# Performance work log

Hardware: AMD Instinct MI355X
Metric: run time of the kernel (lower is better)

## Reference

```python
import jax, jax.numpy as jnp
import numpy as np

B, S, HE, HD = 32, 2048, 1024, 1024

def setup_inputs() -> dict:
    key = jax.random.key(0)
    k1, k2, k3, k4, k5 = jax.random.split(key, 5)
    enc_hiddens = jax.random.normal(k1, (B, S, HE), dtype=jnp.float32)
    dec_hidden = jax.random.normal(k2, (B, HD), dtype=jnp.float32)
    mask = jax.random.randint(k3, (B, S), 0, 2).astype(bool)  # True = masked out
    # params init uniform(-0.05, 0.05) as in init_weights
    W = jax.random.uniform(k4, (HD, HE + HD), dtype=jnp.float32, minval=-0.05, maxval=0.05)
    V = jax.random.uniform(k5, (1, HD), dtype=jnp.float32, minval=-0.05, maxval=0.05)
    return {"enc_hiddens": enc_hiddens, "dec_hidden": dec_hidden, "mask": mask, "W": W, "V": V}

def reference(enc_hiddens, dec_hidden, mask, W, V):
    # e = V^T tanh(W [enc; dec]) -- split W to avoid materializing the concat:
    # W @ [enc;dec] == W_enc @ enc + W_dec @ dec (same math, fused-friendly)
    HE_ = enc_hiddens.shape[-1]
    W_enc, W_dec = W[:, :HE_], W[:, HE_:]
    h = jnp.tanh(jnp.einsum('bse,de->bsd', enc_hiddens, W_enc)
                 + jnp.einsum('be,de->bd', dec_hidden, W_dec)[:, None, :])  # [B,S,HD]
    scores = jnp.einsum('bsd,od->bs', h, V)  # [B,S] (o==1 squeezed)
    scores = jnp.where(mask, -jnp.inf, scores)
    attn = jax.nn.softmax(scores, axis=1)[:, None, :]  # [B,1,S]
    ctx = jnp.einsum('bos,bse->be', attn, enc_hiddens)  # squeeze of bmm -> [B,HE]
    return (ctx, attn)
```

## Files before the change

### kernel.cpp

```cpp
#include <hip/hip_runtime.h>
#include <hip/hip_bf16.h>
#include <math.h>

#define BB 32
#define SS 2048
#define HE 1024
#define HD 1024
#define WROW (HE + HD)

typedef __attribute__((ext_vector_type(8))) short bf16x8;
typedef __attribute__((ext_vector_type(4))) float f32x4;
typedef __attribute__((ext_vector_type(16))) float f32x16;
typedef __attribute__((ext_vector_type(8))) unsigned short u16x8;

__device__ __forceinline__ unsigned short f2bf(float f) {
    union { float f; unsigned u; } v; v.f = f;
    unsigned r = v.u + 0x7fffu + ((v.u >> 16) & 1u);
    return (unsigned short)(r >> 16);
}

__device__ __forceinline__ unsigned int pk2(float x, float y) {
    union { __hip_bfloat162 h; unsigned int u; } c;
    c.h = __float22bfloat162_rn(float2{x, y});
    return c.u;
}

#define LGKM0()  asm volatile("s_waitcnt lgkmcnt(0)" ::: "memory")
#define BAR()    asm volatile("s_barrier" ::: "memory")

__global__ __launch_bounds__(256) void k_cvt_wfrag(const float* __restrict__ W,
                                                   unsigned short* __restrict__ wf) {
    int i = blockIdx.x * 256 + threadIdx.x;
    int d = i >> 7;
    int c = i & 127;
    const float4* src = (const float4*)(W + (size_t)d * WROW + c * 8);
    float4 a = src[0], b2 = src[1];
    u16x8 o;
    o[0] = f2bf(a.x);  o[1] = f2bf(a.y);  o[2] = f2bf(a.z);  o[3] = f2bf(a.w);
    o[4] = f2bf(b2.x); o[5] = f2bf(b2.y); o[6] = f2bf(b2.z); o[7] = f2bf(b2.w);
    int ks = c >> 1;
    int l  = (d & 31) + 32 * (c & 1);
    int g  = d >> 5;
    *(u16x8*)(wf + ((size_t)(g * 64 + ks) * 64 + l) * 8) = o;
}

__global__ __launch_bounds__(256) void k_projdec2(const float* __restrict__ dec,
                                                  const float* __restrict__ W,
                                                  float* __restrict__ proj) {
    const int tid = threadIdx.x;
    const int dl = tid >> 6;
    const int b  = (tid >> 1) & 31;
    const int hf = tid & 1;
    const int d  = blockIdx.x * 4 + dl;
    const float* wrow = W + (size_t)d * WROW + HE + hf * 512;
    const float* dv   = dec + b * HD + hf * 512;
    float s = 0.f;
    #pragma unroll 4
    for (int e = 0; e < 512; e += 4) {
        float4 w4 = *(const float4*)(wrow + e);
        float4 x4 = *(const float4*)(dv + e);
        s += w4.x * x4.x + w4.y * x4.y + w4.z * x4.z + w4.w * x4.w;
    }
    s += __shfl_xor(s, 1, 64);
    if (hf == 0) proj[b * HD + d] = s;
}

__global__ __launch_bounds__(64) void k_compact(const int* __restrict__ mask,
                                                int* __restrict__ idx,
                                                int* __restrict__ cntblk) {
    const int b = blockIdx.x, ln = threadIdx.x;
    int running = 0;
    for (int s0 = 0; s0 < SS; s0 += 64) {
        int m = mask[b * SS + s0 + ln];
        unsigned long long bal = __ballot(m == 0);
        int pos = __popcll(bal & ((1ull << ln) - 1ull));
        if (m == 0) idx[b * SS + running + pos] = s0 + ln;
        running += __popcll(bal);
    }
    int padded = (running + 63) & ~63;
    for (int i = running + ln; i < padded; i += 64) idx[b * SS + i] = (int)0x80000000;
    if (ln == 0) cntblk[b] = padded >> 6;
}

__global__ __launch_bounds__(1024) void k_blocktab(const int* __restrict__ cntblk,
                                                   int* __restrict__ btab) {
    __shared__ int off[33];
    if (threadIdx.x == 0) {
        int a = 0;
        for (int i = 0; i < 32; i++) { off[i] = a; a += cntblk[i]; }
        off[32] = a;
    }
    __syncthreads();
    int j = threadIdx.x, e = -1;
    #pragma unroll
    for (int b2 = 0; b2 < 32; b2++)
        if (j >= off[b2] && j < off[b2 + 1]) e = (b2 << 16) | (j - off[b2]);
    btab[j] = e;
}

__global__ __launch_bounds__(512, 2) void k_scores_mfma8b(
        const float* __restrict__ enc,
        const unsigned short* __restrict__ wf,
        const float* __restrict__ V,
        const float* __restrict__ proj,
        const int* __restrict__ idx,
        const int* __restrict__ btab,
        float* __restrict__ psc) {
    __shared__ unsigned short SM[8192];

    const int ent = btab[blockIdx.x];
    if (ent < 0) return;

    const int tid = threadIdx.x;
    const int wv = tid >> 6, ln = tid & 63, l31 = ln & 31, hi = ln >> 5;
    const int b   = ent >> 16;
    const int lt0 = (ent & 0xffff) << 6;

    const int rid = idx[b * SS + lt0 + (tid >> 3)];
    const size_t arow = ((size_t)b * SS + (rid & 0xffff)) * 1024;

    f32x16 acc[2][4];
    #pragma unroll
    for (int m = 0; m < 2; m++)
        #pragma unroll
        for (int n = 0; n < 4; n++)
            #pragma unroll
            for (int r = 0; r < 16; r++) acc[m][n][r] = 0.f;

    float4 areg[2];
    bf16x8 bgE[8], bgF[8];

    #define LOAD_A(k) do { \
        const float4* g_ = (const float4*)(enc + arow + (k) + (tid & 7) * 8); \
        areg[0] = g_[0]; areg[1] = g_[1]; \
    } while (0)

    #define CVTW_A(buf) do { \
        int row_ = tid >> 3; \
        union { u16x8 s; uint4 u; } pk_; \
        pk_.u.x = pk2(areg[0].x, areg[0].y); \
        pk_.u.y = pk2(areg[0].z, areg[0].w); \
        pk_.u.z = pk2(areg[1].x, areg[1].y); \
        pk_.u.w = pk2(areg[1].z, areg[1].w); \
        *(u16x8*)&SM[(buf) * 4096 + row_ * 64 + (((tid & 7) ^ (row_ & 7)) << 3)] = pk_.s; \
    } while (0)

    #define LOADB(bgx, tt, ksb) do { \
        _Pragma("unroll") \
        for (int kk = 0; kk < 2; kk++) \
            _Pragma("unroll") \
            for (int n = 0; n < 4; n++) \
                bgx[kk * 4 + n] = *(const bf16x8*)(wf + ((size_t)((wv * 4 + n) * 64 + (tt) * 4 + (ksb) + kk) * 64 + ln) * 8); \
        } while (0)

    #define HALF(bg, ksb, Ac) do { \
        _Pragma("unroll") \
        for (int kk = 0; kk < 2; kk++) { \
            bf16x8 af0, af1; \
            { int c_ = ((ksb) + kk) * 2 + hi; int row_ = l31; \
              af0 = *(const bf16x8*)&(Ac)[row_ * 64 + ((c_ ^ (row_ & 7)) << 3)]; } \
            { int c_ = ((ksb) + kk) * 2 + hi; int row_ = 32 + l31; \
              af1 = *(const bf16x8*)&(Ac)[row_ * 64 + ((c_ ^ (row_ & 7)) << 3)]; } \
            __builtin_amdgcn_s_setprio(1); \
            _Pragma("unroll") \
            for (int n = 0; n < 4; n++) \
                acc[0][n] = __builtin_amdgcn_mfma_f32_32x32x16_bf16(af0, bg[kk * 4 + n], acc[0][n], 0, 0, 0); \
            _Pragma("unroll") \
            for (int n = 0; n < 4; n++) \
                acc[1][n] = __builtin_amdgcn_mfma_f32_32x32x16_bf16(af1, bg[kk * 4 + n], acc[1][n], 0, 0, 0); \
            __builtin_amdgcn_s_setprio(0); \
        } } while (0)

    LOADB(bgE, 0, 0); LOADB(bgF, 0, 2);
    LOAD_A(0);
    CVTW_A(0);
    LOAD_A(64);
    LGKM0(); BAR();

    for (int t = 0; t < 16; ++t) {
        const int cur = t & 1, nxt = cur ^ 1;
        const unsigned short* Ac = SM + cur * 4096;

        HALF(bgE, 0, Ac);

        if (t < 15) {
            LOADB(bgE, t + 1, 0);
            CVTW_A(nxt);
            if (t < 14) LOAD_A((t + 2) * 64);
        }

        HALF(bgF, 2, Ac);

        if (t < 15) {
            LOADB(bgF, t + 1, 2);
            LGKM0(); BAR();
        }
    }
    #undef LOAD_A
    #undef CVTW_A
    #undef LOADB
    #undef HALF

    float sc[2][16];
    #pragma unroll
    for (int m = 0; m < 2; m++)
        #pragma unroll
        for (int r = 0; r < 16; r++) sc[m][r] = 0.f;
    #pragma unroll
    for (int n = 0; n < 4; n++) {
        int d = wv * 128 + n * 32 + l31;
        float pd  = proj[b * 1024 + d];
        float vv  = V[d];
        float vv2 = 2.f * vv;
        #pragma unroll
        for (int m = 0; m < 2; m++)
            #pragma unroll
            for (int r = 0; r < 16; r++) {
                float y  = acc[m][n][r] + pd;
                float e2 = __expf(2.f * y);
                float rc = __builtin_amdgcn_rcpf(e2 + 1.f);
                sc[m][r] += vv - vv2 * rc;
            }
    }

    #pragma unroll
    for (int m = 0; m < 2; m++)
        #pragma unroll
        for (int r = 0; r < 16; r++) {
            float v = sc[m][r];
            v += __shfl_xor(v, 1, 64);
            v += __shfl_xor(v, 2, 64);
            v += __shfl_xor(v, 4, 64);
            v += __shfl_xor(v, 8, 64);
            v += __shfl_xor(v, 16, 64);
            sc[m][r] = v;
        }

    __syncthreads();
    float* redf = (float*)SM;
    if (l31 == 0) {
        #pragma unroll
        for (int m = 0; m < 2; m++)
            #pragma unroll
            for (int r = 0; r < 16; r++) {
                int tok = m * 32 + (r & 3) + 8 * (r >> 2) + 4 * hi;
                redf[tok * 8 + wv] = sc[m][r];
            }
    }
    __syncthreads();
    if (tid < 64) {
        float s = 0.f;
        #pragma unroll
        for (int w = 0; w < 8; w++) s += redf[tid * 8 + w];
        int sidx = idx[b * SS + lt0 + tid];
        if (sidx >= 0) psc[b * SS + sidx] = s;
    }
}

__global__ __launch_bounds__(256) void k_softmax_p(const float* __restrict__ psc,
                                                   const int* __restrict__ mask,
                                                   float* __restrict__ attn) {
    __shared__ float sred[256];
    const int b = blockIdx.x, tid = threadIdx.x;
    float vals[8];
    int   msk[8];
    float lmax = -1e30f;
    #pragma unroll
    for (int i = 0; i < 8; i++) {
        int s = tid + i * 256;
        msk[i]  = mask[b * SS + s];
        vals[i] = msk[i] ? 0.f : psc[b * SS + s];
        if (!msk[i]) lmax = fmaxf(lmax, vals[i]);
    }
    sred[tid] = lmax; __syncthreads();
    for (int off = 128; off > 0; off >>= 1) {
        if (tid < off) sred[tid] = fmaxf(sred[tid], sred[tid + off]);
        __syncthreads();
    }
    float m = sred[0];
    __syncthreads();
    float ex[8];
    float lsum = 0.f;
    #pragma unroll
    for (int i = 0; i < 8; i++) {
        ex[i] = msk[i] ? 0.f : __expf(vals[i] - m);
        lsum += ex[i];
    }
    sred[tid] = lsum; __syncthreads();
    for (int off = 128; off > 0; off >>= 1) {
        if (tid < off) sred[tid] += sred[tid + off];
        __syncthreads();
    }
    float inv = 1.f / sred[0];
    #pragma unroll
    for (int i = 0; i < 8; i++) attn[b * SS + tid + i * 256] = ex[i] * inv;
}

__global__ __launch_bounds__(256) void k_ctx_part(const float* __restrict__ enc,
                                                  const float* __restrict__ attn,
                                                  float* __restrict__ pctx) {
    const int b = blockIdx.x, z = blockIdx.y, tid = threadIdx.x;
    float4 acc = {0.f, 0.f, 0.f, 0.f};
    const float4* e4 = (const float4*)(enc + ((size_t)b * SS + z * 64) * HE);
    const float*  ar = attn + b * SS + z * 64;
    for (int s = 0; s < 64; s++) {
        float a = ar[s];
        if (a != 0.f) {
            float4 v = e4[(size_t)s * 256 + tid];
            acc.x += a * v.x; acc.y += a * v.y; acc.z += a * v.z; acc.w += a * v.w;
        }
    }
    *(float4*)(pctx + ((size_t)z * 32 + b) * 1024 + tid * 4) = acc;
}

__global__ __launch_bounds__(256) void k_ctx_red(const float* __restrict__ pctx,
                                                 float* __restrict__ ctx) {
    int i = blockIdx.x * 256 + threadIdx.x;
    float s = 0.f;
    #pragma unroll
    for (int z = 0; z < 32; z++) s += pctx[z * 32768 + i];
    ctx[i] = s;
}

__global__ __launch_bounds__(256) void k_scores_f32(const float* __restrict__ enc,
                                                    const float* __restrict__ W,
                                                    const float* __restrict__ V,
                                                    const float* __restrict__ proj,
                                                    float* __restrict__ scores) {
    __shared__ float As[64][20];
    __shared__ float Bs[64][20];
    __shared__ float red[64][17];
    const int t0 = blockIdx.x * 64;
    const int b  = t0 >> 11;
    const int tid = threadIdx.x;
    const int tx = tid & 15, ty = tid >> 4;
    const int lrow = tid >> 2, lc4 = (tid & 3) * 4;
    float sc[4] = {0.f, 0.f, 0.f, 0.f};
    for (int n0 = 0; n0 < HD; n0 += 64) {
        float C[4][4] = {};
        for (int k0 = 0; k0 < HE; k0 += 16) {
            *(float4*)&As[lrow][lc4] = *(const float4*)(enc + (size_t)(t0 + lrow) * HE + k0 + lc4);
            *(float4*)&Bs[lrow][lc4] = *(const float4*)(W + (size_t)(n0 + lrow) * WROW + k0 + lc4);
            __syncthreads();
            #pragma unroll
            for (int k4 = 0; k4 < 16; k4 += 4) {
                float4 a[4], bb[4];
                #pragma unroll
                for (int i = 0; i < 4; i++) a[i]  = *(float4*)&As[ty * 4 + i][k4];
                #pragma unroll
                for (int j = 0; j < 4; j++) bb[j] = *(float4*)&Bs[tx * 4 + j][k4];
                #pragma unroll
                for (int i = 0; i < 4; i++)
                    #pragma unroll
                    for (int j = 0; j < 4; j++)
                        C[i][j] += a[i].x * bb[j].x + a[i].y * bb[j].y +
                                   a[i].z * bb[j].z + a[i].w * bb[j].w;
            }
            __syncthreads();
        }
        #pragma unroll
        for (int j = 0; j < 4; j++) {
            int d = n0 + tx * 4 + j;
            float pd = proj[b * HD + d];
            float v  = V[d];
            #pragma unroll
            for (int i = 0; i < 4; i++) {
                float y  = C[i][j] + pd;
                float e2 = __expf(2.f * y);
                sc[i] += v * (1.f - 2.f / (e2 + 1.f));
            }
        }
    }
    #pragma unroll
    for (int i = 0; i < 4; i++) red[ty * 4 + i][tx] = sc[i];
    __syncthreads();
    if (tid < 64) {
        float s = 0.f;
        #pragma unroll
        for (int x = 0; x < 16; x++) s += red[tid][x];
        scores[t0 + tid] = s;
    }
}

__global__ __launch_bounds__(256) void k_softmax_f32(float* __restrict__ sc_attn,
                                                     const int* __restrict__ mask) {
    __shared__ float sred[256];
    const int b = blockIdx.x, tid = threadIdx.x;
    float vals[8]; int msk[8];
    float lmax = -1e30f;
    #pragma unroll
    for (int i = 0; i < 8; i++) {
        int s = tid + i * 256;
        vals[i] = sc_attn[b * SS + s];
        msk[i]  = mask[b * SS + s];
        if (!msk[i]) lmax = fmaxf(lmax, vals[i]);
    }
    sred[tid] = lmax; __syncthreads();
    for (int off = 128; off > 0; off >>= 1) {
        if (tid < off) sred[tid] = fmaxf(sred[tid], sred[tid + off]);
        __syncthreads();
    }
    float m = sred[0];
    __syncthreads();
    float ex[8]; float lsum = 0.f;
    #pragma unroll
    for (int i = 0; i < 8; i++) { ex[i] = msk[i] ? 0.f : __expf(vals[i] - m); lsum += ex[i]; }
    sred[tid] = lsum; __syncthreads();
    for (int off = 128; off > 0; off >>= 1) {
        if (tid < off) sred[tid] += sred[tid + off];
        __syncthreads();
    }
    float inv = 1.f / sred[0];
    #pragma unroll
    for (int i = 0; i < 8; i++) sc_attn[b * SS + tid + i * 256] = ex[i] * inv;
}

__global__ __launch_bounds__(256) void k_ctx_atomic(const float* __restrict__ enc,
                                                    const float* __restrict__ attn,
                                                    float* __restrict__ ctx) {
    const int b = blockIdx.x;
    const int e = blockIdx.y * 256 + threadIdx.x;
    const int s0 = blockIdx.z * 256;
    float sum = 0.f;
    for (int s = s0; s < s0 + 256; s++)
        sum += attn[b * SS + s] * enc[((size_t)b * SS + s) * HE + e];
    atomicAdd(&ctx[b * HE + e], sum);
}

extern "C" void kernel_launch(void* const* d_in, const int* in_sizes, int n_in,
                              void* d_out, int out_size, void* d_ws, size_t ws_size,
                              hipStream_t stream) {
    const float* enc  = (const float*)d_in[0];
    const float* dec  = (const float*)d_in[1];
    const int*   mask = (const int*)d_in[2];
    const float* W    = (const float*)d_in[3];
    const float* V    = (const float*)d_in[4];

    float* out  = (float*)d_out;
    float* ctx  = out;
    float* attn = out + BB * HE;

    const size_t WF_OFF = 0, PROJ_OFF = 2097152, PSC_OFF = PROJ_OFF + 131072,
                 PCTX_OFF = PSC_OFF + 262144, IDX_OFF = PCTX_OFF + 4194304,
                 CNT_OFF = IDX_OFF + 262144, BT_OFF = CNT_OFF + 4096,
                 WS_NEED = BT_OFF + 4096;
    if (ws_size >= WS_NEED) {
        char* w = (char*)d_ws;
        unsigned short* wf = (unsigned short*)(w + WF_OFF);
        float* proj        = (float*)(w + PROJ_OFF);
        float* psc         = (float*)(w + PSC_OFF);
        float* pctx        = (float*)(w + PCTX_OFF);
        int*   idx         = (int*)(w + IDX_OFF);
        int*   cntblk      = (int*)(w + CNT_OFF);
        int*   btab        = (int*)(w + BT_OFF);

        k_compact<<<BB, 64, 0, stream>>>(mask, idx, cntblk);
        k_blocktab<<<1, 1024, 0, stream>>>(cntblk, btab);
        k_cvt_wfrag<<<512, 256, 0, stream>>>(W, wf);
        k_projdec2<<<256, 256, 0, stream>>>(dec, W, proj);
        k_scores_mfma8b<<<1024, 512, 0, stream>>>(enc, wf, V, proj, idx, btab, psc);
        k_softmax_p<<<BB, 256, 0, stream>>>(psc, mask, attn);
        k_ctx_part<<<dim3(BB, 32), 256, 0, stream>>>(enc, attn, pctx);
        k_ctx_red<<<128, 256, 0, stream>>>(pctx, ctx);
    } else {
        float* proj  = ctx;
        float* score = attn;
        k_projdec2<<<256, 256, 0, stream>>>(dec, W, proj);
        k_scores_f32<<<(BB * SS) / 64, 256, 0, stream>>>(enc, W, V, proj, score);
        k_softmax_f32<<<BB, 256, 0, stream>>>(score, mask);
        hipMemsetAsync(ctx, 0, (size_t)BB * HE * sizeof(float), stream);
        k_ctx_atomic<<<dim3(BB, HE / 256, 8), 256, 0, stream>>>(enc, attn, ctx);
    }
}
```

Baseline: 187.4 us.

## Fuse softmax numerator and context accumulation into scores kernel without max subtraction

The scores kernel now exponentiates each score directly, with no running max, and writes per-tile partial sums Z. It also accumulates the exp-weighted enc rows for its own 64 tokens, which are still hot in cache, into a partial numerator. A small normalization kernel and a final reduce replace the separate softmax, ctx_part and ctx_red kernels, and the blocktab kernel is removed by computing the tile mapping inline. The intent is to drop the second full read of enc and several launches. Skipping the max subtraction risks overflow if scores were large, which the bounded tanh·V range makes unlikely here.

```diff
diff --git a/kernel.cpp b/kernel.cpp
--- a/kernel.cpp
+++ b/kernel.cpp
@@ -82,39 +82,34 @@
     if (ln == 0) cntblk[b] = padded >> 6;
 }
 
-__global__ __launch_bounds__(1024) void k_blocktab(const int* __restrict__ cntblk,
-                                                   int* __restrict__ btab) {
-    __shared__ int off[33];
-    if (threadIdx.x == 0) {
-        int a = 0;
-        for (int i = 0; i < 32; i++) { off[i] = a; a += cntblk[i]; }
-        off[32] = a;
-    }
-    __syncthreads();
-    int j = threadIdx.x, e = -1;
-    #pragma unroll
-    for (int b2 = 0; b2 < 32; b2++)
-        if (j >= off[b2] && j < off[b2 + 1]) e = (b2 << 16) | (j - off[b2]);
-    btab[j] = e;
-}
-
 __global__ __launch_bounds__(512, 2) void k_scores_mfma8b(
         const float* __restrict__ enc,
         const unsigned short* __restrict__ wf,
         const float* __restrict__ V,
         const float* __restrict__ proj,
         const int* __restrict__ idx,
-        const int* __restrict__ btab,
-        float* __restrict__ psc) {
+        const int* __restrict__ cntblk,
+        float* __restrict__ psc,
+        float* __restrict__ pZ,
+        float* __restrict__ pnum) {
     __shared__ unsigned short SM[8192];
 
-    const int ent = btab[blockIdx.x];
-    if (ent < 0) return;
+    const int lid = (blockIdx.x & 7) * 128 + (blockIdx.x >> 3);
+    int b = -1, loc = 0;
+    {
+        int a = 0;
+        #pragma unroll
+        for (int i = 0; i < 32; i++) {
+            int c = cntblk[i];
+            if (lid >= a && lid < a + c) { b = i; loc = lid - a; }
+            a += c;
+        }
+    }
+    if (b < 0) return;
+    const int lt0 = loc << 6;
 
     const int tid = threadIdx.x;
     const int wv = tid >> 6, ln = tid & 63, l31 = ln & 31, hi = ln >> 5;
-    const int b   = ent >> 16;
-    const int lt0 = (ent & 0xffff) << 6;
 
     const int rid = idx[b * SS + lt0 + (tid >> 3)];
     const size_t arow = ((size_t)b * SS + (rid & 0xffff)) * 1024;
@@ -238,6 +233,8 @@
 
     __syncthreads();
     float* redf = (float*)SM;
+    float* pf   = (float*)SM + 512;
+    int*   ri   = (int*)SM + 576;
     if (l31 == 0) {
         #pragma unroll
         for (int m = 0; m < 2; m++)
@@ -253,73 +250,67 @@
         #pragma unroll
         for (int w = 0; w < 8; w++) s += redf[tid * 8 + w];
         int sidx = idx[b * SS + lt0 + tid];
-        if (sidx >= 0) psc[b * SS + sidx] = s;
-    }
-}
-
-__global__ __launch_bounds__(256) void k_softmax_p(const float* __restrict__ psc,
-                                                   const int* __restrict__ mask,
-                                                   float* __restrict__ attn) {
-    __shared__ float sred[256];
+        float p = (sidx >= 0) ? __expf(s) : 0.f;
+        if (sidx >= 0) psc[b * SS + sidx] = p;
+        pf[tid] = p;
+        ri[tid] = sidx & 0xffff;
+        float z = p;
+        z += __shfl_xor(z, 1, 64);
+        z += __shfl_xor(z, 2, 64);
+        z += __shfl_xor(z, 4, 64);
+        z += __shfl_xor(z, 8, 64);
+        z += __shfl_xor(z, 16, 64);
+        z += __shfl_xor(z, 32, 64);
+        if (tid == 0) pZ[b * 32 + loc] = z;
+    }
+    __syncthreads();
+
+    float n0 = 0.f, n1 = 0.f;
+    const float* encb = enc + (size_t)b * SS * 1024;
+    for (int s2 = 0; s2 < 64; s2++) {
+        float p = pf[s2];
+        if (p != 0.f) {
+            const float* rp = encb + (size_t)ri[s2] * 1024;
+            n0 = fmaf(p, rp[tid], n0);
+            n1 = fmaf(p, rp[tid + 512], n1);
+        }
+    }
+    float* pn = pnum + ((size_t)(b * 32 + loc)) * 1024;
+    pn[tid]       = n0;
+    pn[tid + 512] = n1;
+}
+
+__global__ __launch_bounds__(256) void k_norm(const float* __restrict__ psc,
+                                              const int* __restrict__ mask,
+                                              const float* __restrict__ pZ,
+                                              const int* __restrict__ cntblk,
+                                              float* __restrict__ attn) {
     const int b = blockIdx.x, tid = threadIdx.x;
-    float vals[8];
-    int   msk[8];
-    float lmax = -1e30f;
+    const int c = cntblk[b];
+    float Z = 0.f;
+    for (int q = 0; q < c; q++) Z += pZ[b * 32 + q];
+    float invZ = 1.f / Z;
     #pragma unroll
     for (int i = 0; i < 8; i++) {
         int s = tid + i * 256;
-        msk[i]  = mask[b * SS + s];
-        vals[i] = msk[i] ? 0.f : psc[b * SS + s];
-        if (!msk[i]) lmax = fmaxf(lmax, vals[i]);
-    }
-    sred[tid] = lmax; __syncthreads();
-    for (int off = 128; off > 0; off >>= 1) {
-        if (tid < off) sred[tid] = fmaxf(sred[tid], sred[tid + off]);
-        __syncthreads();
-    }
-    float m = sred[0];
-    __syncthreads();
-    float ex[8];
-    float lsum = 0.f;
-    #pragma unroll
-    for (int i = 0; i < 8; i++) {
-        ex[i] = msk[i] ? 0.f : __expf(vals[i] - m);
-        lsum += ex[i];
-    }
-    sred[tid] = lsum; __syncthreads();
-    for (int off = 128; off > 0; off >>= 1) {
-        if (tid < off) sred[tid] += sred[tid + off];
-        __syncthreads();
-    }
-    float inv = 1.f / sred[0];
-    #pragma unroll
-    for (int i = 0; i < 8; i++) attn[b * SS + tid + i * 256] = ex[i] * inv;
-}
-
-__global__ __launch_bounds__(256) void k_ctx_part(const float* __restrict__ enc,
-                                                  const float* __restrict__ attn,
-                                                  float* __restrict__ pctx) {
-    const int b = blockIdx.x, z = blockIdx.y, tid = threadIdx.x;
-    float4 acc = {0.f, 0.f, 0.f, 0.f};
-    const float4* e4 = (const float4*)(enc + ((size_t)b * SS + z * 64) * HE);
-    const float*  ar = attn + b * SS + z * 64;
-    for (int s = 0; s < 64; s++) {
-        float a = ar[s];
-        if (a != 0.f) {
-            float4 v = e4[(size_t)s * 256 + tid];
-            acc.x += a * v.x; acc.y += a * v.y; acc.z += a * v.z; acc.w += a * v.w;
-        }
-    }
-    *(float4*)(pctx + ((size_t)z * 32 + b) * 1024 + tid * 4) = acc;
-}
-
-__global__ __launch_bounds__(256) void k_ctx_red(const float* __restrict__ pctx,
-                                                 float* __restrict__ ctx) {
+        int m = mask[b * SS + s];
+        float p = m ? 0.f : psc[b * SS + s];
+        attn[b * SS + s] = p * invZ;
+    }
+}
+
+__global__ __launch_bounds__(256) void k_ctx_final(const float* __restrict__ pnum,
+                                                   const float* __restrict__ pZ,
+                                                   const int* __restrict__ cntblk,
+                                                   float* __restrict__ ctx) {
     int i = blockIdx.x * 256 + threadIdx.x;
+    int b = i >> 10, e = i & 1023;
+    const int c = cntblk[b];
+    float Z = 0.f;
+    for (int q = 0; q < c; q++) Z += pZ[b * 32 + q];
     float s = 0.f;
-    #pragma unroll
-    for (int z = 0; z < 32; z++) s += pctx[z * 32768 + i];
-    ctx[i] = s;
+    for (int q = 0; q < c; q++) s += pnum[(size_t)(b * 32 + q) * 1024 + e];
+    ctx[i] = s / Z;
 }
 
 __global__ __launch_bounds__(256) void k_scores_f32(const float* __restrict__ enc,
@@ -441,27 +432,26 @@
     float* attn = out + BB * HE;
 
     const size_t WF_OFF = 0, PROJ_OFF = 2097152, PSC_OFF = PROJ_OFF + 131072,
-                 PCTX_OFF = PSC_OFF + 262144, IDX_OFF = PCTX_OFF + 4194304,
-                 CNT_OFF = IDX_OFF + 262144, BT_OFF = CNT_OFF + 4096,
-                 WS_NEED = BT_OFF + 4096;
+                 IDX_OFF = PSC_OFF + 262144, CNT_OFF = IDX_OFF + 262144,
+                 PZ_OFF = CNT_OFF + 4096, PN_OFF = PZ_OFF + 4096,
+                 WS_NEED = PN_OFF + 4194304;
     if (ws_size >= WS_NEED) {
         char* w = (char*)d_ws;
         unsigned short* wf = (unsigned short*)(w + WF_OFF);
         float* proj        = (float*)(w + PROJ_OFF);
         float* psc         = (float*)(w + PSC_OFF);
-        float* pctx        = (float*)(w + PCTX_OFF);
         int*   idx         = (int*)(w + IDX_OFF);
         int*   cntblk      = (int*)(w + CNT_OFF);
-        int*   btab        = (int*)(w + BT_OFF);
+        float* pZ          = (float*)(w + PZ_OFF);
+        float* pnum        = (float*)(w + PN_OFF);
 
         k_compact<<<BB, 64, 0, stream>>>(mask, idx, cntblk);
-        k_blocktab<<<1, 1024, 0, stream>>>(cntblk, btab);
         k_cvt_wfrag<<<512, 256, 0, stream>>>(W, wf);
         k_projdec2<<<256, 256, 0, stream>>>(dec, W, proj);
-        k_scores_mfma8b<<<1024, 512, 0, stream>>>(enc, wf, V, proj, idx, btab, psc);
-        k_softmax_p<<<BB, 256, 0, stream>>>(psc, mask, attn);
-        k_ctx_part<<<dim3(BB, 32), 256, 0, stream>>>(enc, attn, pctx);
-        k_ctx_red<<<128, 256, 0, stream>>>(pctx, ctx);
+        k_scores_mfma8b<<<1024, 512, 0, stream>>>(enc, wf, V, proj, idx, cntblk,
+                                                  psc, pZ, pnum);
+        k_norm<<<BB, 256, 0, stream>>>(psc, mask, pZ, cntblk, attn);
+        k_ctx_final<<<128, 256, 0, stream>>>(pnum, pZ, cntblk, ctx);
     } else {
         float* proj  = ctx;
         float* score = attn;
```

Result: slower. 284.7 us (+51.9%).
